# Kernel optimization log

Hardware: AMD Instinct MI355X
Metric: run time of the kernel (lower is better)

Reference implementation:

```python
import jax, jax.numpy as jnp
import numpy as np

T = 10          # time_steps
IN_DIM = 784    # 28*28
HID = 256
NCLS = 47
THRESH = 1.0
TAU_MEM = 2.0   # LIF membrane time constant
TAU_OUT = 2.0   # readout EMA time constant


@jax.custom_vjp
def spike_fn(u):
    # Heaviside spike on (v - threshold), surrogate gradient in bwd.
    return (u >= 0.0).astype(u.dtype)

def _spike_fwd(u):
    return spike_fn(u), u

def _spike_bwd(u, g):
    # sigmoid surrogate derivative, slope 4
    s = jax.nn.sigmoid(4.0 * u)
    return (g * 4.0 * s * (1.0 - s),)

spike_fn.defvjp(_spike_fwd, _spike_bwd)


def setup_inputs() -> dict:
    key = jax.random.key(0)
    k1, k2, k3 = jax.random.split(key, 3)
    x = jax.random.uniform(k1, (4096, 1, 28, 28), dtype=jnp.float32)
    W1 = jax.random.normal(k2, (IN_DIM, HID), dtype=jnp.float32) / np.float32(np.sqrt(IN_DIM))
    b1 = jnp.zeros((HID,), jnp.float32)
    Wr = jax.random.normal(k3, (HID, NCLS), dtype=jnp.float32) / np.float32(np.sqrt(HID))
    br = jnp.zeros((NCLS,), jnp.float32)
    return {"x": x, "W1": W1, "b1": b1, "Wr": Wr, "br": br}


def reference(x, W1, b1, Wr, br):
    B = x.shape[0]
    xf = x.reshape(B, -1)  # [B, 784] pixel intensities in [0,1]
    # rate_encode_flat: Bernoulli(p=pixel) spikes per timestep -> [T, B, 784]
    ek = jax.random.key(42)
    seq = (jax.random.uniform(ek, (T, B, IN_DIM), dtype=xf.dtype) < xf[None]).astype(xf.dtype)

    def step(carry, s_t):
        v_hid, v_out = carry
        I_hid = s_t @ W1 + b1                      # [B, HID]
        v_hid = v_hid + (I_hid - v_hid) / TAU_MEM  # leaky integration
        spk = spike_fn(v_hid - THRESH)             # spike emission
        v_hid = v_hid * (1.0 - spk)                # hard reset to 0
        I = spk @ Wr + br                          # [B, NCLS]
        v_out = v_out + (I - v_out) / TAU_OUT      # output EMA
        return (v_hid, v_out), None

    init = (jnp.zeros((B, HID), xf.dtype), jnp.zeros((B, NCLS), xf.dtype))
    (_, v_out), _ = jax.lax.scan(step, init, seq)
    return v_out
```

## Files before the change

### kernel.cpp

```cpp
#include <hip/hip_runtime.h>
#include <stdint.h>


#define T_STEPS 10
#define BATCH   4096
#define IN_DIM  784
#define HID     256
#define NCLS    47
#define KWORDS  25
#define KPAD    800

#define WS_W1HI_OFF 46039040u
#define WS_W1MD_OFF (46039040u + 409600u)
#define WS_W1LO_OFF (46039040u + 819200u)

typedef __attribute__((ext_vector_type(8))) short    bf16x8;
typedef __attribute__((ext_vector_type(4))) float    f32x4;

__device__ __forceinline__ uint32_t rotl32(uint32_t x, uint32_t r) {
    return __builtin_amdgcn_alignbit(x, x, 32u - r);
}

__device__ __forceinline__ uint32_t tf_hash(uint32_t lo) {
    const uint32_t ks1 = 42u;
    const uint32_t ks2 = 0x1BD11BDAu ^ 42u;
    uint32_t x0 = 0u;
    uint32_t x1 = lo + ks1;
#define TF_RND(r) { x0 += x1; x1 = rotl32(x1, r); x1 ^= x0; }
    TF_RND(13) TF_RND(15) TF_RND(26) TF_RND(6)
    x0 += ks1; x1 += ks2 + 1u;
    TF_RND(17) TF_RND(29) TF_RND(16) TF_RND(24)
    x0 += ks2; x1 += 2u;
    TF_RND(13) TF_RND(15) TF_RND(26) TF_RND(6)
    x1 += ks1 + 3u;
    TF_RND(17) TF_RND(29) TF_RND(16) TF_RND(24)
    x0 += ks1; x1 += ks2 + 4u;
    TF_RND(13) TF_RND(15) TF_RND(26) TF_RND(6)
    x0 += ks2; x1 += 5u;
#undef TF_RND
    return x0 ^ x1;
}

__global__ __launch_bounds__(256) void splitk_k(
        const float* __restrict__ W1, ushort* __restrict__ hiT,
        ushort* __restrict__ midT, ushort* __restrict__ loT) {
    int n = blockIdx.x;
    for (int k = threadIdx.x; k < KPAD; k += 256) {
        float w = (k < IN_DIM) ? W1[k * HID + n] : 0.0f;
        uint32_t u = __float_as_uint(w);
        uint32_t hb = (u + 0x7FFFu + ((u >> 16) & 1u)) >> 16;
        float hf = __uint_as_float(hb << 16);
        float r1 = w - hf;
        uint32_t u1 = __float_as_uint(r1);
        uint32_t mb = (u1 + 0x7FFFu + ((u1 >> 16) & 1u)) >> 16;
        float mf2 = __uint_as_float(mb << 16);
        float r2 = r1 - mf2;
        uint32_t u2 = __float_as_uint(r2);
        uint32_t lb = (u2 + 0x7FFFu + ((u2 >> 16) & 1u)) >> 16;
        hiT [n * KPAD + k] = (ushort)hb;
        midT[n * KPAD + k] = (ushort)mb;
        loT [n * KPAD + k] = (ushort)lb;
    }
}

#define A_BUFSZ 5120
#define LDS_B0  10240
#define G_LDW   260

__global__ __launch_bounds__(512, 4) void fused_gemm_k(
        const ushort* __restrict__ hiT, const ushort* __restrict__ midT,
        const ushort* __restrict__ loT, const float* __restrict__ b1,
        const float* __restrict__ x, const float* __restrict__ Wr,
        const float* __restrict__ br, float* __restrict__ out) {
    __shared__ __align__(16) char lds[59392];

    const int tid = threadIdx.x;
    const int l   = tid & 63;
    const int wv  = tid >> 6;
    const int b0  = blockIdx.x << 3;

    f32x4 acc[5][2] = {};

    const int q   = l >> 4;
    const int c0  = l & 15;
    const int sig = q ^ (l & 3) ^ ((l >> 2) & 3);
    const int a_rd = (c0 << 6) + (sig << 4);
    const int b_rd = (wv << 11) + (c0 << 6) + (sig << 4);

    const ushort* hi_p[2];
    const ushort* md_p[2];
    const ushort* lo_p[2];
    int bdst[2];
#pragma unroll
    for (int i = 0; i < 2; ++i) {
        int s  = (i << 9) + tid;
        int n  = s >> 2;
        int qs = s & 3;
        int qd = qs ^ (n & 3) ^ ((n >> 2) & 3);
        size_t eoff = (size_t)n * KPAD + ((size_t)qd << 3);
        hi_p[i] = hiT  + eoff;
        md_p[i] = midT + eoff;
        lo_p[i] = loT  + eoff;
        bdst[i] = ((i << 9) + (wv << 6)) << 4;
    }

    const int eL = tid & 31;
    int      adst[5];
    int      xoff[5];
    uint32_t tib[5];
#pragma unroll
    for (int s = 0; s < 5; ++s) {
        int tau = tid + (s << 9);
        int row = tau >> 5;
        int p   = eL >> 1;
        int qd  = (p >> 2) ^ (row & 3) ^ ((row >> 2) & 3);
        adst[s] = (row << 6) + (qd << 4) + ((p & 3) << 2) + ((eL & 1) << 1);
        int j   = row & 7;
        int t   = row >> 3;
        int rowg = t * BATCH + b0 + j;
        xoff[s] = (b0 + j) * IN_DIM + eL;
        tib[s]  = (uint32_t)rowg * (uint32_t)IN_DIM + (uint32_t)eL;
    }

#define STAGE_B(koff) \
    _Pragma("unroll") \
    for (int i = 0; i < 2; ++i) { \
        __builtin_amdgcn_global_load_lds( \
            (const __attribute__((address_space(1))) void*)(hi_p[i] + (koff)), \
            (__attribute__((address_space(3))) void*)(lds + LDS_B0 + bdst[i]), \
            16, 0, 0); \
        __builtin_amdgcn_global_load_lds( \
            (const __attribute__((address_space(1))) void*)(md_p[i] + (koff)), \
            (__attribute__((address_space(3))) void*)(lds + LDS_B0 + 16384 + bdst[i]), \
            16, 0, 0); \
        __builtin_amdgcn_global_load_lds( \
            (const __attribute__((address_space(1))) void*)(lo_p[i] + (koff)), \
            (__attribute__((address_space(3))) void*)(lds + LDS_B0 + 32768 + bdst[i]), \
            16, 0, 0); \
    }

#define HASH_SLAB(koff, abase, is_tail) \
    _Pragma("unroll") \
    for (int s = 0; s < 5; ++s) { \
        ushort w_ = 0; \
        if (!(is_tail) || eL < 16) { \
            float    xs = x[xoff[s] + (koff)] * 8388608.0f; \
            uint32_t h  = tf_hash(tib[s] + (uint32_t)(koff)); \
            if ((float)(h >> 9) < xs) w_ = (ushort)0x3F80; \
        } \
        *(ushort*)(lds + (abase) + adst[s]) = w_; \
    }

#define PRELOAD_FRAGS(bufidx) \
    const char* A = lds + (bufidx) * A_BUFSZ; \
    bf16x8 af[5]; \
    bf16x8 bfr[3][2]; \
    _Pragma("unroll") \
    for (int mt = 0; mt < 5; ++mt) \
        af[mt] = *(const bf16x8*)(A + a_rd + (mt << 10)); \
    _Pragma("unroll") \
    for (int nt = 0; nt < 2; ++nt) { \
        bfr[0][nt] = *(const bf16x8*)(lds + LDS_B0 + b_rd + (nt << 10)); \
        bfr[1][nt] = *(const bf16x8*)(lds + LDS_B0 + 16384 + b_rd + (nt << 10)); \
        bfr[2][nt] = *(const bf16x8*)(lds + LDS_B0 + 32768 + b_rd + (nt << 10)); \
    }

#define MFMA_ALL \
    _Pragma("unroll") \
    for (int nt = 0; nt < 2; ++nt) { \
        _Pragma("unroll") \
        for (int mt = 0; mt < 5; ++mt) { \
            acc[mt][nt] = __builtin_amdgcn_mfma_f32_16x16x32_bf16(af[mt], bfr[0][nt], acc[mt][nt], 0, 0, 0); \
            acc[mt][nt] = __builtin_amdgcn_mfma_f32_16x16x32_bf16(af[mt], bfr[1][nt], acc[mt][nt], 0, 0, 0); \
            acc[mt][nt] = __builtin_amdgcn_mfma_f32_16x16x32_bf16(af[mt], bfr[2][nt], acc[mt][nt], 0, 0, 0); \
        } \
    }

    STAGE_B(0)
    HASH_SLAB(0, 0, false)
    __syncthreads();

    int cur = 0;
#pragma unroll 1
    for (int kw = 0; kw < KWORDS; ++kw) {
        {
            PRELOAD_FRAGS(cur)
            if (kw < KWORDS - 1) {
                const int koff = (kw + 1) << 5;
                if (kw == KWORDS - 2) { HASH_SLAB(koff, (cur ^ 1) * A_BUFSZ, true) }
                else                  { HASH_SLAB(koff, (cur ^ 1) * A_BUFSZ, false) }
            }
            MFMA_ALL
        }
        __syncthreads();
        if (kw < KWORDS - 1) {
            STAGE_B((kw + 1) << 5)
            __syncthreads();
        }
        cur ^= 1;
    }
#undef STAGE_B
#undef HASH_SLAB
#undef PRELOAD_FRAGS
#undef MFMA_ALL

    float b1v[2];
#pragma unroll
    for (int nt = 0; nt < 2; ++nt)
        b1v[nt] = b1[(wv << 5) + (nt << 4) + c0];

    float av[5][2][4];
#pragma unroll
    for (int mt = 0; mt < 5; ++mt)
#pragma unroll
        for (int nt = 0; nt < 2; ++nt)
#pragma unroll
            for (int rr = 0; rr < 4; ++rr)
                av[mt][nt][rr] = acc[mt][nt][rr] + b1v[nt];

    const int qh = q >> 1;
    float g[2][4];
#pragma unroll
    for (int nt = 0; nt < 2; ++nt) {
#pragma unroll
        for (int rr = 0; rr < 4; ++rr) {
            float v = 0.f, ga = 0.f, wt = 0.0009765625f;
#pragma unroll
            for (int m = 0; m < 5; ++m) {
                float pv = __shfl_xor(av[m][nt][rr], 32);
                float Ie = qh ? pv : av[m][nt][rr];
                float Io = qh ? av[m][nt][rr] : pv;
                v = v + (Ie - v) * 0.5f;
                if (v >= 1.0f) { ga += wt; v = 0.f; }
                wt += wt;
                v = v + (Io - v) * 0.5f;
                if (v >= 1.0f) { ga += wt; v = 0.f; }
                wt += wt;
            }
            g[nt][rr] = ga;
        }
    }

    float* gbuf = (float*)lds;
    if (l < 32) {
#pragma unroll
        for (int nt = 0; nt < 2; ++nt)
#pragma unroll
            for (int rr = 0; rr < 4; ++rr) {
                int j   = ((q & 1) << 2) + rr;
                int col = (wv << 5) + (nt << 4) + c0;
                gbuf[j * G_LDW + col] = g[nt][rr];
            }
    }
    __syncthreads();

    {
        const int c = l;
        if (c < NCLS) {
            const float* gb = &gbuf[wv * G_LDW];
            float a = 0.f;
            for (int h4 = 0; h4 < 64; ++h4) {
                float w0 = Wr[((h4 << 2) + 0) * NCLS + c];
                float w1 = Wr[((h4 << 2) + 1) * NCLS + c];
                float w2 = Wr[((h4 << 2) + 2) * NCLS + c];
                float w3 = Wr[((h4 << 2) + 3) * NCLS + c];
                float4 gg = *(const float4*)&gb[h4 << 2];
                a = fmaf(gg.x, w0, a);
                a = fmaf(gg.y, w1, a);
                a = fmaf(gg.z, w2, a);
                a = fmaf(gg.w, w3, a);
            }
            out[(b0 + wv) * NCLS + c] = a + br[c] * 0.9990234375f;
        }
    }
}

extern "C" void kernel_launch(void* const* d_in, const int* in_sizes, int n_in,
                              void* d_out, int out_size, void* d_ws, size_t ws_size,
                              hipStream_t stream) {
    const float* x  = (const float*)d_in[0];
    const float* W1 = (const float*)d_in[1];
    const float* b1 = (const float*)d_in[2];
    const float* Wr = (const float*)d_in[3];
    const float* br = (const float*)d_in[4];
    float* out = (float*)d_out;

    ushort* w1hi  = (ushort*)((char*)d_ws + WS_W1HI_OFF);
    ushort* w1md  = (ushort*)((char*)d_ws + WS_W1MD_OFF);
    ushort* w1lo  = (ushort*)((char*)d_ws + WS_W1LO_OFF);

    splitk_k<<<HID, 256, 0, stream>>>(W1, w1hi, w1md, w1lo);
    fused_gemm_k<<<BATCH / 8, 512, 0, stream>>>(w1hi, w1md, w1lo, b1, x,
                                                Wr, br, out);
}
```

Before: 176.7 us.

## Load W1 fragments directly from global in MFMA-ready layout, drop LDS staging

The split-bf16 W1 preprocessing now writes the hi/mid/lo planes in a k-word-major, fragment-contiguous layout. The GEMM kernel then loads B fragments straight from global memory into registers instead of staging them through LDS with global_load_lds. This removes the B staging area from shared memory (59KB down to 10KB, which could allow more resident blocks) and one barrier per k-step. The cost is that each wave issues its own global loads for B, relying on L2/L1 hits, with latency that is less hidden. The A hashing address math is also simplified to constant offsets.

```diff
diff --git a/kernel.cpp b/kernel.cpp
--- a/kernel.cpp
+++ b/kernel.cpp
@@ -57,14 +57,15 @@
         float r2 = r1 - mf2;
         uint32_t u2 = __float_as_uint(r2);
         uint32_t lb = (u2 + 0x7FFFu + ((u2 >> 16) & 1u)) >> 16;
-        hiT [n * KPAD + k] = (ushort)hb;
-        midT[n * KPAD + k] = (ushort)mb;
-        loT [n * KPAD + k] = (ushort)lb;
+        int kw = k >> 5, qk = (k >> 3) & 3, j = k & 7;
+        size_t o = ((size_t)(kw * 256 + n) * 4 + qk) * 8 + j;
+        hiT [o] = (ushort)hb;
+        midT[o] = (ushort)mb;
+        loT [o] = (ushort)lb;
     }
 }
 
 #define A_BUFSZ 5120
-#define LDS_B0  10240
 #define G_LDW   260
 
 __global__ __launch_bounds__(512, 4) void fused_gemm_k(
@@ -72,7 +73,7 @@
         const ushort* __restrict__ loT, const float* __restrict__ b1,
         const float* __restrict__ x, const float* __restrict__ Wr,
         const float* __restrict__ br, float* __restrict__ out) {
-    __shared__ __align__(16) char lds[59392];
+    __shared__ __align__(16) char lds[10240];
 
     const int tid = threadIdx.x;
     const int l   = tid & 63;
@@ -85,85 +86,46 @@
     const int c0  = l & 15;
     const int sig = q ^ (l & 3) ^ ((l >> 2) & 3);
     const int a_rd = (c0 << 6) + (sig << 4);
-    const int b_rd = (wv << 11) + (c0 << 6) + (sig << 4);
-
-    const ushort* hi_p[2];
-    const ushort* md_p[2];
-    const ushort* lo_p[2];
-    int bdst[2];
-#pragma unroll
-    for (int i = 0; i < 2; ++i) {
-        int s  = (i << 9) + tid;
-        int n  = s >> 2;
-        int qs = s & 3;
-        int qd = qs ^ (n & 3) ^ ((n >> 2) & 3);
-        size_t eoff = (size_t)n * KPAD + ((size_t)qd << 3);
-        hi_p[i] = hiT  + eoff;
-        md_p[i] = midT + eoff;
-        lo_p[i] = loT  + eoff;
-        bdst[i] = ((i << 9) + (wv << 6)) << 4;
-    }
-
-    const int eL = tid & 31;
-    int      adst[5];
-    int      xoff[5];
-    uint32_t tib[5];
-#pragma unroll
-    for (int s = 0; s < 5; ++s) {
-        int tau = tid + (s << 9);
-        int row = tau >> 5;
-        int p   = eL >> 1;
-        int qd  = (p >> 2) ^ (row & 3) ^ ((row >> 2) & 3);
-        adst[s] = (row << 6) + (qd << 4) + ((p & 3) << 2) + ((eL & 1) << 1);
-        int j   = row & 7;
-        int t   = row >> 3;
-        int rowg = t * BATCH + b0 + j;
-        xoff[s] = (b0 + j) * IN_DIM + eL;
-        tib[s]  = (uint32_t)rowg * (uint32_t)IN_DIM + (uint32_t)eL;
-    }
-
-#define STAGE_B(koff) \
-    _Pragma("unroll") \
-    for (int i = 0; i < 2; ++i) { \
-        __builtin_amdgcn_global_load_lds( \
-            (const __attribute__((address_space(1))) void*)(hi_p[i] + (koff)), \
-            (__attribute__((address_space(3))) void*)(lds + LDS_B0 + bdst[i]), \
-            16, 0, 0); \
-        __builtin_amdgcn_global_load_lds( \
-            (const __attribute__((address_space(1))) void*)(md_p[i] + (koff)), \
-            (__attribute__((address_space(3))) void*)(lds + LDS_B0 + 16384 + bdst[i]), \
-            16, 0, 0); \
-        __builtin_amdgcn_global_load_lds( \
-            (const __attribute__((address_space(1))) void*)(lo_p[i] + (koff)), \
-            (__attribute__((address_space(3))) void*)(lds + LDS_B0 + 32768 + bdst[i]), \
-            16, 0, 0); \
-    }
-
-#define HASH_SLAB(koff, abase, is_tail) \
+
+    const int beoff = ((wv << 5) + c0) * 32 + (q << 3);
+    const ushort* bp_hi = hiT  + beoff;
+    const ushort* bp_md = midT + beoff;
+    const ushort* bp_lo = loT  + beoff;
+
+    const int eL   = tid & 31;
+    const int row0 = tid >> 5;
+    const int j0   = row0 & 7;
+    const int qd0  = ((eL >> 1) >> 2) ^ (row0 & 3) ^ ((row0 >> 2) & 3);
+    const int adst0 = (row0 << 6) + (qd0 << 4) + (((eL >> 1) & 3) << 2)
+                    + ((eL & 1) << 1);
+    const int xbase = (b0 + j0) * IN_DIM + eL;
+    const uint32_t tib0 = (uint32_t)((row0 >> 3) * BATCH + b0 + j0)
+                        * (uint32_t)IN_DIM + (uint32_t)eL;
+
+#define HASH_SLAB(koff, abase, xv) \
     _Pragma("unroll") \
     for (int s = 0; s < 5; ++s) { \
-        ushort w_ = 0; \
-        if (!(is_tail) || eL < 16) { \
-            float    xs = x[xoff[s] + (koff)] * 8388608.0f; \
-            uint32_t h  = tf_hash(tib[s] + (uint32_t)(koff)); \
-            if ((float)(h >> 9) < xs) w_ = (ushort)0x3F80; \
-        } \
-        *(ushort*)(lds + (abase) + adst[s]) = w_; \
-    }
-
-#define PRELOAD_FRAGS(bufidx) \
+        uint32_t h = tf_hash(tib0 + (uint32_t)(s * 6422528) + (uint32_t)(koff)); \
+        ushort w_ = ((float)(h >> 9) < (xv) * 8388608.0f) ? (ushort)0x3F80 : (ushort)0; \
+        *(ushort*)(lds + (abase) + adst0 + (s << 10)) = w_; \
+    }
+
+#define PRELOAD_A(bufidx) \
     const char* A = lds + (bufidx) * A_BUFSZ; \
     bf16x8 af[5]; \
+    _Pragma("unroll") \
+    for (int mt = 0; mt < 5; ++mt) \
+        af[mt] = *(const bf16x8*)(A + a_rd + (mt << 10));
+
+#define LOAD_B \
     bf16x8 bfr[3][2]; \
     _Pragma("unroll") \
-    for (int mt = 0; mt < 5; ++mt) \
-        af[mt] = *(const bf16x8*)(A + a_rd + (mt << 10)); \
-    _Pragma("unroll") \
     for (int nt = 0; nt < 2; ++nt) { \
-        bfr[0][nt] = *(const bf16x8*)(lds + LDS_B0 + b_rd + (nt << 10)); \
-        bfr[1][nt] = *(const bf16x8*)(lds + LDS_B0 + 16384 + b_rd + (nt << 10)); \
-        bfr[2][nt] = *(const bf16x8*)(lds + LDS_B0 + 32768 + b_rd + (nt << 10)); \
-    }
+        bfr[0][nt] = *(const bf16x8*)(bp_hi + nt * 512); \
+        bfr[1][nt] = *(const bf16x8*)(bp_md + nt * 512); \
+        bfr[2][nt] = *(const bf16x8*)(bp_lo + nt * 512); \
+    } \
+    bp_hi += 8192; bp_md += 8192; bp_lo += 8192;
 
 #define MFMA_ALL \
     _Pragma("unroll") \
@@ -176,32 +138,32 @@
         } \
     }
 
-    STAGE_B(0)
-    HASH_SLAB(0, 0, false)
+    {
+        float xv0 = x[xbase];
+        HASH_SLAB(0, 0, xv0)
+    }
     __syncthreads();
 
     int cur = 0;
 #pragma unroll 1
     for (int kw = 0; kw < KWORDS; ++kw) {
-        {
-            PRELOAD_FRAGS(cur)
-            if (kw < KWORDS - 1) {
-                const int koff = (kw + 1) << 5;
-                if (kw == KWORDS - 2) { HASH_SLAB(koff, (cur ^ 1) * A_BUFSZ, true) }
-                else                  { HASH_SLAB(koff, (cur ^ 1) * A_BUFSZ, false) }
-            }
-            MFMA_ALL
+        LOAD_B
+        PRELOAD_A(cur)
+        if (kw < KWORDS - 1) {
+            const int koff = (kw + 1) << 5;
+            float xv = 0.0f;
+            if (!(kw == KWORDS - 2 && eL >= 16))
+                xv = x[xbase + koff];
+            HASH_SLAB(koff, (cur ^ 1) * A_BUFSZ, xv)
         }
+        MFMA_ALL
+
         __syncthreads();
-        if (kw < KWORDS - 1) {
-            STAGE_B((kw + 1) << 5)
-            __syncthreads();
-        }
         cur ^= 1;
     }
-#undef STAGE_B
 #undef HASH_SLAB
-#undef PRELOAD_FRAGS
+#undef PRELOAD_A
+#undef LOAD_B
 #undef MFMA_ALL
 
     float b1v[2];
@@ -247,9 +209,9 @@
         for (int nt = 0; nt < 2; ++nt)
 #pragma unroll
             for (int rr = 0; rr < 4; ++rr) {
-                int j   = ((q & 1) << 2) + rr;
+                int jj  = ((q & 1) << 2) + rr;
                 int col = (wv << 5) + (nt << 4) + c0;
-                gbuf[j * G_LDW + col] = g[nt][rr];
+                gbuf[jj * G_LDW + col] = g[nt][rr];
             }
     }
     __syncthreads();
```

Result: no change. 178.6 us (+1.1%).
